# Performance work log

Measured on AMD Instinct MI355X. Metric: run time of the kernel, lower is better.

Reference implementation:

```python
import jax, jax.numpy as jnp
import numpy as np

B, T, N, H, P = 16, 64, 512, 128, 12


def _laplacian_with_self_loop(adj):
    a = adj + jnp.eye(adj.shape[0], dtype=adj.dtype)
    d_inv_sqrt = 1.0 / jnp.sqrt(a.sum(axis=1))
    return a * d_inv_sqrt[:, None] * d_inv_sqrt[None, :]


def setup_inputs() -> dict:
    key = jax.random.key(0)
    ks = jax.random.split(key, 10)
    inputs = jax.random.normal(ks[0], (B, T, N), dtype=jnp.float32)
    adj = jax.random.uniform(ks[1], (N, N), dtype=jnp.float32)
    adj = (adj + adj.T) * 0.5
    laplacian = _laplacian_with_self_loop(adj)

    def xavier(k, shape):
        fan_in, fan_out = shape[0], shape[1]
        lim = np.sqrt(6.0 / (fan_in + fan_out))
        return jax.random.uniform(k, shape, jnp.float32, -lim, lim)

    W1 = xavier(ks[2], (H + 1, 2 * H))      # graph_conv1 weights
    b1 = jnp.ones((2 * H,), jnp.float32)    # bias init 1.0
    W2 = xavier(ks[3], (H + 1, H))          # graph_conv2 weights
    b2 = jnp.zeros((H,), jnp.float32)
    att_w1 = xavier(ks[4], (H, 1))
    att_w2 = xavier(ks[5], (N, 1))
    att_w3 = xavier(ks[6], (N, 1))
    att_b1 = jnp.zeros((1,), jnp.float32)
    att_b2 = jnp.zeros((1,), jnp.float32)
    att_b3 = jnp.zeros((1,), jnp.float32)
    W_out = xavier(ks[7], (T, P))
    b_out = jnp.zeros((P,), jnp.float32)
    return dict(inputs=inputs, laplacian=laplacian, W1=W1, b1=b1, W2=W2, b2=b2,
                att_w1=att_w1, att_w2=att_w2, att_w3=att_w3,
                att_b1=att_b1, att_b2=att_b2, att_b3=att_b3,
                W_out=W_out, b_out=b_out)


def reference(inputs, laplacian, W1, b1, W2, b2,
              att_w1, att_w2, att_w3, att_b1, att_b2, att_b3,
              W_out, b_out):
    Bs, Ts, Ns = inputs.shape
    Hs = W2.shape[1]

    def graph_conv(x_t, h_flat, W, b):
        # x_t: [B,N]; h_flat: [B, N*H]
        h = h_flat.reshape(Bs, Ns, Hs)
        conc = jnp.concatenate([x_t[..., None], h], axis=-1)     # [B,N,H+1]
        agg = jnp.einsum('mn,bnc->bmc', laplacian, conc)          # [B,N,H+1]
        out = agg @ W + b                                         # [B,N,O]
        return out.reshape(Bs, -1)                                # [B,N*O] (flattened, matching torch)

    def step(h_flat, x_t):
        ru = jax.nn.sigmoid(graph_conv(x_t, h_flat, W1, b1))      # [B, N*2H]
        r, u = jnp.split(ru, 2, axis=1)                            # split on flattened dim (faithful)
        c = jnp.tanh(graph_conv(x_t, r * h_flat, W2, b2))          # [B, N*H]
        new_h = u * h_flat + (1.0 - u) * c
        return new_h, new_h

    h0 = jnp.zeros((Bs, Ns * Hs), inputs.dtype)
    _, hs = jax.lax.scan(step, h0, jnp.moveaxis(inputs, 1, 0))     # [T,B,N*H]
    hidden_states = jnp.moveaxis(hs, 0, 1).reshape(Bs, Ts, Ns, Hs)

    # SelfAttention: project H->1, then N->1 per (b,t), softmax over T
    hs1 = hidden_states.reshape(-1, Hs) @ att_w1 + att_b1          # [B*T*N, 1]
    f = (hs1.reshape(-1, Ns) @ att_w2 + att_b2).reshape(Bs, Ts)
    g = (hs1.reshape(-1, Ns) @ att_w3 + att_b3).reshape(Bs, Ts)
    beta = jax.nn.softmax(g * f, axis=-1)                          # [B,T]
    context = beta[:, :, None] * hs1.reshape(Bs, Ts, Ns)           # [B,T,N]

    context = context.transpose(0, 2, 1)                           # [B,N,T]
    Ps = W_out.shape[1]
    out = (context.reshape(-1, Ts) @ W_out + b_out).reshape(Bs, Ns, Ps)
    return out.transpose(0, 2, 1)                                  # [B,pre_len,N]
```

## Files before the change

kernel.cpp:

```cpp
#include <hip/hip_runtime.h>
#include <math.h>

#define B_ 16
#define T_ 64
#define N_ 512
#define H_ 128
#define P_ 12
#define NH 65536

__global__ __launch_bounds__(512) void lx_kernel(const float* __restrict__ x,
                                                 const float* __restrict__ L,
                                                 float* __restrict__ Lx) {
    __shared__ __align__(16) float xs[4][N_];
    const int r0 = blockIdx.x * 4;
    const int tid = threadIdx.x;
    for (int j = 0; j < 4; ++j)
        xs[j][tid] = x[(size_t)(r0 + j) * N_ + tid];
    __syncthreads();
    float a0 = 0.f, a1 = 0.f, a2 = 0.f, a3 = 0.f;
    const int m = tid;
#pragma unroll 8
    for (int n = 0; n < N_; ++n) {
        float lv = L[(size_t)n * N_ + m];
        a0 += xs[0][n] * lv;
        a1 += xs[1][n] * lv;
        a2 += xs[2][n] * lv;
        a3 += xs[3][n] * lv;
    }
    Lx[(size_t)(r0 + 0) * N_ + m] = a0;
    Lx[(size_t)(r0 + 1) * N_ + m] = a1;
    Lx[(size_t)(r0 + 2) * N_ + m] = a2;
    Lx[(size_t)(r0 + 3) * N_ + m] = a3;
}

__global__ __launch_bounds__(512) void gc1_kernel(
    const float* __restrict__ L, const float* __restrict__ Hprev,
    const float* __restrict__ Lx, const float* __restrict__ W1,
    const float* __restrict__ b1, float* __restrict__ rh,
    float* __restrict__ u, int t) {
    __shared__ __align__(16) float Ht[2][32][H_];
    union LW {
        float Lt[2][32][33];
        float Wt[16][260];
    };
    __shared__ __align__(16) LW sm;
    __shared__ __align__(16) float Zb[32][H_];

    const int tid = threadIdx.x;
    const int b = blockIdx.x & 15;
    const int m0 = (blockIdx.x >> 4) * 32;
    const float* __restrict__ Hb = Hprev + (size_t)b * NH;

    const int hrow = tid >> 5, hcol = (tid & 31) * 4;
    const int lm = tid >> 4, lk0 = (tid & 15) * 2;

    {
        *(float4*)&Ht[0][hrow][hcol] = *(const float4*)&Hb[(size_t)hrow * H_ + hcol];
        *(float4*)&Ht[0][hrow + 16][hcol] =
            *(const float4*)&Hb[(size_t)(hrow + 16) * H_ + hcol];
        float2 lv = *(const float2*)&L[(size_t)(m0 + lm) * N_ + lk0];
        sm.Lt[0][lk0 + 0][lm] = lv.x;
        sm.Lt[0][lk0 + 1][lm] = lv.y;
    }
    __syncthreads();

    const int g = tid >> 8;
    const int gt = tid & 255;
    const int tx = gt & 31, ty = gt >> 5;
    const int c0 = tx * 4, mrow = ty * 4;

    float acc[4][4] = {};

    for (int kc = 0; kc < 16; ++kc) {
        const int bi = kc & 1, bj = bi ^ 1;
        float4 p0, p1;
        float2 pl;
        if (kc < 15) {
            const size_t kb = (size_t)(kc + 1) * 32;
            p0 = *(const float4*)&Hb[(kb + hrow) * H_ + hcol];
            p1 = *(const float4*)&Hb[(kb + hrow + 16) * H_ + hcol];
            pl = *(const float2*)&L[(size_t)(m0 + lm) * N_ + kb + lk0];
        }
#pragma unroll
        for (int kk = 0; kk < 16; ++kk) {
            const int k = g * 16 + kk;
            const float4 la = *(const float4*)&sm.Lt[bi][k][mrow];
            const float4 hv = *(const float4*)&Ht[bi][k][c0];
            acc[0][0] += la.x * hv.x; acc[0][1] += la.x * hv.y;
            acc[0][2] += la.x * hv.z; acc[0][3] += la.x * hv.w;
            acc[1][0] += la.y * hv.x; acc[1][1] += la.y * hv.y;
            acc[1][2] += la.y * hv.z; acc[1][3] += la.y * hv.w;
            acc[2][0] += la.z * hv.x; acc[2][1] += la.z * hv.y;
            acc[2][2] += la.z * hv.z; acc[2][3] += la.z * hv.w;
            acc[3][0] += la.w * hv.x; acc[3][1] += la.w * hv.y;
            acc[3][2] += la.w * hv.z; acc[3][3] += la.w * hv.w;
        }
        if (kc < 15) {
            *(float4*)&Ht[bj][hrow][hcol] = p0;
            *(float4*)&Ht[bj][hrow + 16][hcol] = p1;
            sm.Lt[bj][lk0 + 0][lm] = pl.x;
            sm.Lt[bj][lk0 + 1][lm] = pl.y;
        }
        __syncthreads();
    }

    if (g == 1) {
#pragma unroll
        for (int i = 0; i < 4; ++i)
            *(float4*)&Zb[mrow + i][c0] =
                make_float4(acc[i][0], acc[i][1], acc[i][2], acc[i][3]);
    }
    __syncthreads();
    if (g == 0) {
#pragma unroll
        for (int i = 0; i < 4; ++i) {
            float4 z = *(const float4*)&Zb[mrow + i][c0];
            *(float4*)&Zb[mrow + i][c0] = make_float4(
                acc[i][0] + z.x, acc[i][1] + z.y, acc[i][2] + z.z, acc[i][3] + z.w);
        }
    }
    __syncthreads();

    const int to = tid & 63, tm = tid >> 6;
    const int o0 = to * 4;
    float a2[4][4] = {};
    const int wr = tid >> 5, wc = (tid & 31) * 4;

    for (int ck = 0; ck < 8; ++ck) {
        *(float4*)&sm.Wt[wr][wc] =
            *(const float4*)&W1[(size_t)(1 + ck * 16 + wr) * 256 + wc];
        *(float4*)&sm.Wt[wr][wc + 128] =
            *(const float4*)&W1[(size_t)(1 + ck * 16 + wr) * 256 + wc + 128];
        __syncthreads();
#pragma unroll
        for (int ch4 = 0; ch4 < 4; ++ch4) {
            const float4 w0v = *(const float4*)&sm.Wt[ch4 * 4 + 0][o0];
            const float4 w1v = *(const float4*)&sm.Wt[ch4 * 4 + 1][o0];
            const float4 w2v = *(const float4*)&sm.Wt[ch4 * 4 + 2][o0];
            const float4 w3v = *(const float4*)&sm.Wt[ch4 * 4 + 3][o0];
            const int cc = ck * 16 + ch4 * 4;
#pragma unroll
            for (int i = 0; i < 4; ++i) {
                const float4 zv = *(const float4*)&Zb[tm + 8 * i][cc];
                a2[i][0] += zv.x * w0v.x + zv.y * w1v.x + zv.z * w2v.x + zv.w * w3v.x;
                a2[i][1] += zv.x * w0v.y + zv.y * w1v.y + zv.z * w2v.y + zv.w * w3v.y;
                a2[i][2] += zv.x * w0v.z + zv.y * w1v.z + zv.z * w2v.z + zv.w * w3v.z;
                a2[i][3] += zv.x * w0v.w + zv.y * w1v.w + zv.z * w2v.w + zv.w * w3v.w;
            }
        }
        __syncthreads();
    }

    const float4 w0r = *(const float4*)&W1[o0];
    const float4 bbv = *(const float4*)&b1[o0];
    const float* __restrict__ LxRow = Lx + ((size_t)b * T_ + t) * N_ + m0;
    float* __restrict__ rhB = rh + (size_t)b * NH;
    float* __restrict__ uB = u + (size_t)b * NH;
    const bool isR = (m0 < 256);
#pragma unroll
    for (int i = 0; i < 4; ++i) {
        const int mi = tm + 8 * i;
        const float lx = LxRow[mi];
        float v0 = a2[i][0] + lx * w0r.x + bbv.x;
        float v1 = a2[i][1] + lx * w0r.y + bbv.y;
        float v2 = a2[i][2] + lx * w0r.z + bbv.z;
        float v3 = a2[i][3] + lx * w0r.w + bbv.w;
        float s0 = 1.f / (1.f + expf(-v0));
        float s1 = 1.f / (1.f + expf(-v1));
        float s2 = 1.f / (1.f + expf(-v2));
        float s3 = 1.f / (1.f + expf(-v3));
        const int fl = (m0 + mi) * 256 + o0;
        if (isR) {
            float4 hv = *(const float4*)&Hb[fl];
            *(float4*)&rhB[fl] = make_float4(s0 * hv.x, s1 * hv.y, s2 * hv.z, s3 * hv.w);
        } else {
            *(float4*)&uB[fl - NH] = make_float4(s0, s1, s2, s3);
        }
    }
}

__global__ __launch_bounds__(512) void gc2_kernel(
    const float* __restrict__ L, const float* __restrict__ Hprev,
    const float* __restrict__ rh, const float* __restrict__ u,
    const float* __restrict__ Lx, const float* __restrict__ W2,
    const float* __restrict__ b2, const float* __restrict__ aw1,
    const float* __restrict__ ab1, float* __restrict__ Hnew,
    float* __restrict__ hs1, int t) {
    __shared__ __align__(16) float Ht[2][32][H_];
    union LW {
        float Lt[2][32][33];
        float Wt[16][132];
    };
    __shared__ __align__(16) LW sm;
    __shared__ __align__(16) float Zb[32][H_];
    __shared__ __align__(16) float red[32][32];

    const int tid = threadIdx.x;
    const int b = blockIdx.x & 15;
    const int m0 = (blockIdx.x >> 4) * 32;
    const float* __restrict__ Rb = rh + (size_t)b * NH;
    const float* __restrict__ Hb = Hprev + (size_t)b * NH;
    const float* __restrict__ Ub = u + (size_t)b * NH;

    const int hrow = tid >> 5, hcol = (tid & 31) * 4;
    const int lm = tid >> 4, lk0 = (tid & 15) * 2;

    {
        *(float4*)&Ht[0][hrow][hcol] = *(const float4*)&Rb[(size_t)hrow * H_ + hcol];
        *(float4*)&Ht[0][hrow + 16][hcol] =
            *(const float4*)&Rb[(size_t)(hrow + 16) * H_ + hcol];
        float2 lv = *(const float2*)&L[(size_t)(m0 + lm) * N_ + lk0];
        sm.Lt[0][lk0 + 0][lm] = lv.x;
        sm.Lt[0][lk0 + 1][lm] = lv.y;
    }
    __syncthreads();

    const int g = tid >> 8;
    const int gt = tid & 255;
    const int tx = gt & 31, ty = gt >> 5;
    const int c0 = tx * 4, mrow = ty * 4;

    float acc[4][4] = {};

    for (int kc = 0; kc < 16; ++kc) {
        const int bi = kc & 1, bj = bi ^ 1;
        float4 p0, p1;
        float2 pl;
        if (kc < 15) {
            const size_t kb = (size_t)(kc + 1) * 32;
            p0 = *(const float4*)&Rb[(kb + hrow) * H_ + hcol];
            p1 = *(const float4*)&Rb[(kb + hrow + 16) * H_ + hcol];
            pl = *(const float2*)&L[(size_t)(m0 + lm) * N_ + kb + lk0];
        }
#pragma unroll
        for (int kk = 0; kk < 16; ++kk) {
            const int k = g * 16 + kk;
            const float4 la = *(const float4*)&sm.Lt[bi][k][mrow];
            const float4 hv = *(const float4*)&Ht[bi][k][c0];
            acc[0][0] += la.x * hv.x; acc[0][1] += la.x * hv.y;
            acc[0][2] += la.x * hv.z; acc[0][3] += la.x * hv.w;
            acc[1][0] += la.y * hv.x; acc[1][1] += la.y * hv.y;
            acc[1][2] += la.y * hv.z; acc[1][3] += la.y * hv.w;
            acc[2][0] += la.z * hv.x; acc[2][1] += la.z * hv.y;
            acc[2][2] += la.z * hv.z; acc[2][3] += la.z * hv.w;
            acc[3][0] += la.w * hv.x; acc[3][1] += la.w * hv.y;
            acc[3][2] += la.w * hv.z; acc[3][3] += la.w * hv.w;
        }
        if (kc < 15) {
            *(float4*)&Ht[bj][hrow][hcol] = p0;
            *(float4*)&Ht[bj][hrow + 16][hcol] = p1;
            sm.Lt[bj][lk0 + 0][lm] = pl.x;
            sm.Lt[bj][lk0 + 1][lm] = pl.y;
        }
        __syncthreads();
    }

    if (g == 1) {
#pragma unroll
        for (int i = 0; i < 4; ++i)
            *(float4*)&Zb[mrow + i][c0] =
                make_float4(acc[i][0], acc[i][1], acc[i][2], acc[i][3]);
    }
    __syncthreads();
    if (g == 0) {
#pragma unroll
        for (int i = 0; i < 4; ++i) {
            float4 z = *(const float4*)&Zb[mrow + i][c0];
            *(float4*)&Zb[mrow + i][c0] = make_float4(
                acc[i][0] + z.x, acc[i][1] + z.y, acc[i][2] + z.z, acc[i][3] + z.w);
        }
    }
    __syncthreads();

    const int to = tid & 31, tm = tid >> 5;
    const int o0 = to * 4;
    float a2[2][4] = {};
    const int wr = tid >> 5, wc = (tid & 31) * 4;

    for (int ck = 0; ck < 8; ++ck) {
        *(float4*)&sm.Wt[wr][wc] =
            *(const float4*)&W2[(size_t)(1 + ck * 16 + wr) * H_ + wc];
        __syncthreads();
#pragma unroll
        for (int ch4 = 0; ch4 < 4; ++ch4) {
            const float4 w0v = *(const float4*)&sm.Wt[ch4 * 4 + 0][o0];
            const float4 w1v = *(const float4*)&sm.Wt[ch4 * 4 + 1][o0];
            const float4 w2v = *(const float4*)&sm.Wt[ch4 * 4 + 2][o0];
            const float4 w3v = *(const float4*)&sm.Wt[ch4 * 4 + 3][o0];
            const int cc = ck * 16 + ch4 * 4;
#pragma unroll
            for (int i = 0; i < 2; ++i) {
                const float4 zv = *(const float4*)&Zb[tm + 16 * i][cc];
                a2[i][0] += zv.x * w0v.x + zv.y * w1v.x + zv.z * w2v.x + zv.w * w3v.x;
                a2[i][1] += zv.x * w0v.y + zv.y * w1v.y + zv.z * w2v.y + zv.w * w3v.y;
                a2[i][2] += zv.x * w0v.z + zv.y * w1v.z + zv.z * w2v.z + zv.w * w3v.z;
                a2[i][3] += zv.x * w0v.w + zv.y * w1v.w + zv.z * w2v.w + zv.w * w3v.w;
            }
        }
        __syncthreads();
    }

    const float4 w0r = *(const float4*)&W2[o0];
    const float4 bbv = *(const float4*)&b2[o0];
    const float4 awv = *(const float4*)&aw1[o0];
    const float* __restrict__ LxRow = Lx + ((size_t)b * T_ + t) * N_ + m0;
    float* __restrict__ HnB = Hnew + (size_t)b * NH;
#pragma unroll
    for (int i = 0; i < 2; ++i) {
        const int mi = tm + 16 * i;
        const float lx = LxRow[mi];
        float c0e = tanhf(a2[i][0] + lx * w0r.x + bbv.x);
        float c1e = tanhf(a2[i][1] + lx * w0r.y + bbv.y);
        float c2e = tanhf(a2[i][2] + lx * w0r.z + bbv.z);
        float c3e = tanhf(a2[i][3] + lx * w0r.w + bbv.w);
        const int fl = (m0 + mi) * H_ + o0;
        float4 uv = *(const float4*)&Ub[fl];
        float4 hp = *(const float4*)&Hb[fl];
        float h0 = uv.x * hp.x + (1.f - uv.x) * c0e;
        float h1 = uv.y * hp.y + (1.f - uv.y) * c1e;
        float h2 = uv.z * hp.z + (1.f - uv.z) * c2e;
        float h3 = uv.w * hp.w + (1.f - uv.w) * c3e;
        *(float4*)&HnB[fl] = make_float4(h0, h1, h2, h3);
        red[mi][to] = h0 * awv.x + h1 * awv.y + h2 * awv.z + h3 * awv.w;
    }
    __syncthreads();
    if (tid < 32) {
        float s = 0.f;
#pragma unroll
        for (int k2 = 0; k2 < 32; ++k2) s += red[tid][k2];
        hs1[((size_t)b * T_ + t) * N_ + m0 + tid] = s + ab1[0];
    }
}

__global__ __launch_bounds__(64) void att_beta_kernel(
    const float* __restrict__ hs1, const float* __restrict__ aw2,
    const float* __restrict__ aw3, const float* __restrict__ ab2,
    const float* __restrict__ ab3, float* __restrict__ beta) {
    const int b = blockIdx.x;
    const int t = threadIdx.x;
    const float* __restrict__ row = hs1 + ((size_t)b * T_ + t) * N_;
    float f = 0.f, g = 0.f;
    for (int n = 0; n < N_; n += 4) {
        float4 hv = *(const float4*)&row[n];
        float4 w2v = *(const float4*)&aw2[n];
        float4 w3v = *(const float4*)&aw3[n];
        f += hv.x * w2v.x + hv.y * w2v.y + hv.z * w2v.z + hv.w * w2v.w;
        g += hv.x * w3v.x + hv.y * w3v.y + hv.z * w3v.z + hv.w * w3v.w;
    }
    f += ab2[0];
    g += ab3[0];
    float s = f * g;
    float mx = s;
    for (int off = 32; off; off >>= 1) mx = fmaxf(mx, __shfl_xor(mx, off));
    float e = expf(s - mx);
    float sum = e;
    for (int off = 32; off; off >>= 1) sum += __shfl_xor(sum, off);
    beta[b * T_ + t] = e / sum;
}

__global__ __launch_bounds__(256) void att_out_kernel(
    const float* __restrict__ hs1, const float* __restrict__ beta,
    const float* __restrict__ Wout, const float* __restrict__ bout,
    float* __restrict__ out) {
    __shared__ float bs[T_];
    __shared__ float ws[T_][P_];
    const int b = blockIdx.x;
    const int tid = threadIdx.x;
    if (tid < T_) bs[tid] = beta[b * T_ + tid];
    for (int i = tid; i < T_ * P_; i += 256) ws[i / P_][i % P_] = Wout[i];
    __syncthreads();
    for (int nn = 0; nn < 2; ++nn) {
        const int n = tid + nn * 256;
        float acc[P_];
#pragma unroll
        for (int p = 0; p < P_; ++p) acc[p] = bout[p];
        for (int t = 0; t < T_; ++t) {
            float v = bs[t] * hs1[((size_t)b * T_ + t) * N_ + n];
#pragma unroll
            for (int p = 0; p < P_; ++p) acc[p] += v * ws[t][p];
        }
#pragma unroll
        for (int p = 0; p < P_; ++p) out[((size_t)b * P_ + p) * N_ + n] = acc[p];
    }
}

extern "C" void kernel_launch(void* const* d_in, const int* in_sizes, int n_in,
                              void* d_out, int out_size, void* d_ws, size_t ws_size,
                              hipStream_t stream) {
    const float* x = (const float*)d_in[0];
    const float* L = (const float*)d_in[1];
    const float* W1 = (const float*)d_in[2];
    const float* b1 = (const float*)d_in[3];
    const float* W2 = (const float*)d_in[4];
    const float* b2 = (const float*)d_in[5];
    const float* aw1 = (const float*)d_in[6];
    const float* aw2 = (const float*)d_in[7];
    const float* aw3 = (const float*)d_in[8];
    const float* ab1 = (const float*)d_in[9];
    const float* ab2 = (const float*)d_in[10];
    const float* ab3 = (const float*)d_in[11];
    const float* Wout = (const float*)d_in[12];
    const float* bout = (const float*)d_in[13];
    float* out = (float*)d_out;

    float* ws = (float*)d_ws;
    float* Lx = ws;
    float* hs1 = Lx + B_ * T_ * N_;
    float* hb0 = hs1 + B_ * T_ * N_;
    float* hb1 = hb0 + (size_t)B_ * NH;
    float* rh = hb1 + (size_t)B_ * NH;
    float* u = rh + (size_t)B_ * NH;
    float* beta = u + (size_t)B_ * NH;
    (void)in_sizes; (void)n_in; (void)out_size; (void)ws_size;

    hipMemsetAsync(hb0, 0, (size_t)B_ * NH * sizeof(float), stream);
    lx_kernel<<<256, 512, 0, stream>>>(x, L, Lx);

    for (int t = 0; t < T_; ++t) {
        float* hp = (t & 1) ? hb1 : hb0;
        float* hn = (t & 1) ? hb0 : hb1;
        gc1_kernel<<<256, 512, 0, stream>>>(L, hp, Lx, W1, b1, rh, u, t);
        gc2_kernel<<<256, 512, 0, stream>>>(L, hp, rh, u, Lx, W2, b2, aw1, ab1,
                                            hn, hs1, t);
    }
    att_beta_kernel<<<16, 64, 0, stream>>>(hs1, aw2, aw3, ab2, ab3, beta);
    att_out_kernel<<<16, 256, 0, stream>>>(hs1, beta, Wout, bout, out);
}
```

Baseline: 4.008 ms.

## Use 8x8 register tiles with 8-way K split in graph-conv aggregation

After: 3.823 ms. 1.05x faster.

```diff
diff --git a/kernel.cpp b/kernel.cpp
--- a/kernel.cpp
+++ b/kernel.cpp
@@ -33,6 +33,16 @@
     Lx[(size_t)(r0 + 3) * N_ + m] = a3;
 }
 
+#define FMAQ(u, v, A, Hv)                                                     \
+    acc[u][0][v][0] += (A).x * (Hv).x; acc[u][0][v][1] += (A).x * (Hv).y;     \
+    acc[u][0][v][2] += (A).x * (Hv).z; acc[u][0][v][3] += (A).x * (Hv).w;     \
+    acc[u][1][v][0] += (A).y * (Hv).x; acc[u][1][v][1] += (A).y * (Hv).y;     \
+    acc[u][1][v][2] += (A).y * (Hv).z; acc[u][1][v][3] += (A).y * (Hv).w;     \
+    acc[u][2][v][0] += (A).z * (Hv).x; acc[u][2][v][1] += (A).z * (Hv).y;     \
+    acc[u][2][v][2] += (A).z * (Hv).z; acc[u][2][v][3] += (A).z * (Hv).w;     \
+    acc[u][3][v][0] += (A).w * (Hv).x; acc[u][3][v][1] += (A).w * (Hv).y;     \
+    acc[u][3][v][2] += (A).w * (Hv).z; acc[u][3][v][3] += (A).w * (Hv).w;
+
 __global__ __launch_bounds__(512) void gc1_kernel(
     const float* __restrict__ L, const float* __restrict__ Hprev,
     const float* __restrict__ Lx, const float* __restrict__ W1,
@@ -40,7 +50,7 @@
     float* __restrict__ u, int t) {
     __shared__ __align__(16) float Ht[2][32][H_];
     union LW {
-        float Lt[2][32][33];
+        float Lt[2][32][36];
         float Wt[16][260];
     };
     __shared__ __align__(16) LW sm;
@@ -64,12 +74,14 @@
     }
     __syncthreads();
 
-    const int g = tid >> 8;
-    const int gt = tid & 255;
-    const int tx = gt & 31, ty = gt >> 5;
-    const int c0 = tx * 4, mrow = ty * 4;
-
-    float acc[4][4] = {};
+    const int g = tid >> 6;
+    const int l = tid & 63;
+    const int ty = l >> 4;
+    const int tx = l & 15;
+    const int ma0 = ty * 4, mb0 = 16 + ty * 4;
+    const int ca0 = tx * 4, cb0 = 64 + tx * 4;
+
+    float acc[2][4][2][4] = {};
 
     for (int kc = 0; kc < 16; ++kc) {
         const int bi = kc & 1, bj = bi ^ 1;
@@ -82,18 +94,16 @@
             pl = *(const float2*)&L[(size_t)(m0 + lm) * N_ + kb + lk0];
         }
 #pragma unroll
-        for (int kk = 0; kk < 16; ++kk) {
-            const int k = g * 16 + kk;
-            const float4 la = *(const float4*)&sm.Lt[bi][k][mrow];
-            const float4 hv = *(const float4*)&Ht[bi][k][c0];
-            acc[0][0] += la.x * hv.x; acc[0][1] += la.x * hv.y;
-            acc[0][2] += la.x * hv.z; acc[0][3] += la.x * hv.w;
-            acc[1][0] += la.y * hv.x; acc[1][1] += la.y * hv.y;
-            acc[1][2] += la.y * hv.z; acc[1][3] += la.y * hv.w;
-            acc[2][0] += la.z * hv.x; acc[2][1] += la.z * hv.y;
-            acc[2][2] += la.z * hv.z; acc[2][3] += la.z * hv.w;
-            acc[3][0] += la.w * hv.x; acc[3][1] += la.w * hv.y;
-            acc[3][2] += la.w * hv.z; acc[3][3] += la.w * hv.w;
+        for (int kk = 0; kk < 4; ++kk) {
+            const int k = g * 4 + kk;
+            const float4 la0 = *(const float4*)&sm.Lt[bi][k][ma0];
+            const float4 la1 = *(const float4*)&sm.Lt[bi][k][mb0];
+            const float4 h0 = *(const float4*)&Ht[bi][k][ca0];
+            const float4 h1 = *(const float4*)&Ht[bi][k][cb0];
+            FMAQ(0, 0, la0, h0)
+            FMAQ(0, 1, la0, h1)
+            FMAQ(1, 0, la1, h0)
+            FMAQ(1, 1, la1, h1)
         }
         if (kc < 15) {
             *(float4*)&Ht[bj][hrow][hcol] = p0;
@@ -104,22 +114,32 @@
         __syncthreads();
     }
 
-    if (g == 1) {
-#pragma unroll
-        for (int i = 0; i < 4; ++i)
-            *(float4*)&Zb[mrow + i][c0] =
-                make_float4(acc[i][0], acc[i][1], acc[i][2], acc[i][3]);
-    }
-    __syncthreads();
-    if (g == 0) {
-#pragma unroll
-        for (int i = 0; i < 4; ++i) {
-            float4 z = *(const float4*)&Zb[mrow + i][c0];
-            *(float4*)&Zb[mrow + i][c0] = make_float4(
-                acc[i][0] + z.x, acc[i][1] + z.y, acc[i][2] + z.z, acc[i][3] + z.w);
-        }
-    }
-    __syncthreads();
+    for (int r = 0; r < 8; ++r) {
+        if (g == r) {
+#pragma unroll
+            for (int uu = 0; uu < 2; ++uu)
+#pragma unroll
+                for (int i = 0; i < 4; ++i) {
+                    const int m = uu * 16 + ty * 4 + i;
+#pragma unroll
+                    for (int v = 0; v < 2; ++v) {
+                        const int c = v ? cb0 : ca0;
+                        float4* zp = (float4*)&Zb[m][c];
+                        if (r == 0) {
+                            *zp = make_float4(acc[uu][i][v][0], acc[uu][i][v][1],
+                                              acc[uu][i][v][2], acc[uu][i][v][3]);
+                        } else {
+                            float4 z = *zp;
+                            *zp = make_float4(z.x + acc[uu][i][v][0],
+                                              z.y + acc[uu][i][v][1],
+                                              z.z + acc[uu][i][v][2],
+                                              z.w + acc[uu][i][v][3]);
+                        }
+                    }
+                }
+        }
+        __syncthreads();
+    }
 
     const int to = tid & 63, tm = tid >> 6;
     const int o0 = to * 4;
@@ -188,7 +208,7 @@
     float* __restrict__ hs1, int t) {
     __shared__ __align__(16) float Ht[2][32][H_];
     union LW {
-        float Lt[2][32][33];
+        float Lt[2][32][36];
         float Wt[16][132];
     };
     __shared__ __align__(16) LW sm;
@@ -215,12 +235,14 @@
     }
     __syncthreads();
 
-    const int g = tid >> 8;
-    const int gt = tid & 255;
-    const int tx = gt & 31, ty = gt >> 5;
-    const int c0 = tx * 4, mrow = ty * 4;
-
-    float acc[4][4] = {};
+    const int g = tid >> 6;
+    const int l = tid & 63;
+    const int ty = l >> 4;
+    const int tx = l & 15;
+    const int ma0 = ty * 4, mb0 = 16 + ty * 4;
+    const int ca0 = tx * 4, cb0 = 64 + tx * 4;
+
+    float acc[2][4][2][4] = {};
 
     for (int kc = 0; kc < 16; ++kc) {
         const int bi = kc & 1, bj = bi ^ 1;
@@ -233,18 +255,16 @@
             pl = *(const float2*)&L[(size_t)(m0 + lm) * N_ + kb + lk0];
         }
 #pragma unroll
-        for (int kk = 0; kk < 16; ++kk) {
-            const int k = g * 16 + kk;
-            const float4 la = *(const float4*)&sm.Lt[bi][k][mrow];
-            const float4 hv = *(const float4*)&Ht[bi][k][c0];
-            acc[0][0] += la.x * hv.x; acc[0][1] += la.x * hv.y;
-            acc[0][2] += la.x * hv.z; acc[0][3] += la.x * hv.w;
-            acc[1][0] += la.y * hv.x; acc[1][1] += la.y * hv.y;
-            acc[1][2] += la.y * hv.z; acc[1][3] += la.y * hv.w;
-            acc[2][0] += la.z * hv.x; acc[2][1] += la.z * hv.y;
-            acc[2][2] += la.z * hv.z; acc[2][3] += la.z * hv.w;
-            acc[3][0] += la.w * hv.x; acc[3][1] += la.w * hv.y;
-            acc[3][2] += la.w * hv.z; acc[3][3] += la.w * hv.w;
+        for (int kk = 0; kk < 4; ++kk) {
+            const int k = g * 4 + kk;
+            const float4 la0 = *(const float4*)&sm.Lt[bi][k][ma0];
+            const float4 la1 = *(const float4*)&sm.Lt[bi][k][mb0];
+            const float4 h0 = *(const float4*)&Ht[bi][k][ca0];
+            const float4 h1 = *(const float4*)&Ht[bi][k][cb0];
+            FMAQ(0, 0, la0, h0)
+            FMAQ(0, 1, la0, h1)
+            FMAQ(1, 0, la1, h0)
+            FMAQ(1, 1, la1, h1)
         }
         if (kc < 15) {
             *(float4*)&Ht[bj][hrow][hcol] = p0;
@@ -255,22 +275,32 @@
         __syncthreads();
     }
 
-    if (g == 1) {
-#pragma unroll
-        for (int i = 0; i < 4; ++i)
-            *(float4*)&Zb[mrow + i][c0] =
-                make_float4(acc[i][0], acc[i][1], acc[i][2], acc[i][3]);
-    }
-    __syncthreads();
-    if (g == 0) {
-#pragma unroll
-        for (int i = 0; i < 4; ++i) {
-            float4 z = *(const float4*)&Zb[mrow + i][c0];
-            *(float4*)&Zb[mrow + i][c0] = make_float4(
-                acc[i][0] + z.x, acc[i][1] + z.y, acc[i][2] + z.z, acc[i][3] + z.w);
-        }
-    }
-    __syncthreads();
+    for (int r = 0; r < 8; ++r) {
+        if (g == r) {
+#pragma unroll
+            for (int uu = 0; uu < 2; ++uu)
+#pragma unroll
+                for (int i = 0; i < 4; ++i) {
+                    const int m = uu * 16 + ty * 4 + i;
+#pragma unroll
+                    for (int v = 0; v < 2; ++v) {
+                        const int c = v ? cb0 : ca0;
+                        float4* zp = (float4*)&Zb[m][c];
+                        if (r == 0) {
+                            *zp = make_float4(acc[uu][i][v][0], acc[uu][i][v][1],
+                                              acc[uu][i][v][2], acc[uu][i][v][3]);
+                        } else {
+                            float4 z = *zp;
+                            *zp = make_float4(z.x + acc[uu][i][v][0],
+                                              z.y + acc[uu][i][v][1],
+                                              z.z + acc[uu][i][v][2],
+                                              z.w + acc[uu][i][v][3]);
+                        }
+                    }
+                }
+        }
+        __syncthreads();
+    }
 
     const int to = tid & 31, tm = tid >> 5;
     const int o0 = to * 4;
```
